# Kernel optimization log

Hardware: AMD Instinct MI355X
Metric: run time of the kernel (lower is better)

Reference implementation:

```python
import jax, jax.numpy as jnp
import numpy as np

E, H, M, IN, T = 4, 64, 64, 32, 32      # e_size, hidden_state, message, in_size, target
HL = (128, 256, 128)                     # NNet hidden layers (priba's NNet default)
N_LAYERS = 3


def setup_inputs() -> dict:
    key = jax.random.key(0)
    ks = iter(jax.random.split(key, 64))
    B, N = 16, 128

    def w(shape, scale=0.1):
        return jax.random.normal(next(ks), shape, dtype=jnp.float32) * scale

    inp = {
        "h_in": jax.random.normal(next(ks), (B, N, IN), dtype=jnp.float32),
        "am": jax.random.normal(next(ks), (B, N, N, E), dtype=jnp.float32),
        "g_size": jax.random.randint(next(ks), (B,), 0, N),
    }
    # EdgeNetwork NNet: E -> 128 -> 256 -> 128 -> M*H
    dims_e = (E,) + HL + (M * H,)
    for i in range(4):
        inp[f"We{i}"] = w((dims_e[i], dims_e[i + 1]))
        inp[f"be{i}"] = w((dims_e[i + 1],))
    # GRU (torch nn.GRU, one layer, one step): input M, hidden H
    inp["Wih"] = w((3 * H, M)); inp["Whh"] = w((3 * H, H))
    inp["bih"] = w((3 * H,)); inp["bhh"] = w((3 * H,))
    # Readout NNets: i on [h_T, h_0] (H+IN -> T), j on h_T (H -> T)
    dims_i = (H + IN,) + HL + (T,)
    dims_j = (H,) + HL + (T,)
    for i in range(4):
        inp[f"Wi{i}"] = w((dims_i[i], dims_i[i + 1])); inp[f"bi{i}"] = w((dims_i[i + 1],))
        inp[f"Wj{i}"] = w((dims_j[i], dims_j[i + 1])); inp[f"bj{i}"] = w((dims_j[i + 1],))
    return inp


def _mlp(x, Ws, bs):
    for Wk, bk in zip(Ws[:-1], bs[:-1]):
        x = jax.nn.relu(x @ Wk + bk)
    return x @ Ws[-1] + bs[-1]


def reference(h_in, am, g_size,
              We0, be0, We1, be1, We2, be2, We3, be3,
              Wih, Whh, bih, bhh,
              Wi0, bi0, Wi1, bi1, Wi2, bi2, Wi3, bi3,
              Wj0, bj0, Wj1, bj1, Wj2, bj2, Wj3, bj3):
    B, N, _ = h_in.shape
    h = jnp.pad(h_in, ((0, 0), (0, 0), (0, H - IN)))            # pad to hidden size
    mask = (jnp.arange(N)[None, :] < g_size[:, None]).astype(h.dtype)[:, :, None]  # [B,N,1]

    # Edge-network hidden features; final linear layer is fused into the
    # message contraction to avoid materializing per-edge [M,H] matrices.
    f = am                                                       # [B,N,N,E]
    for Wk, bk in ((We0, be0), (We1, be1), (We2, be2)):
        f = jax.nn.relu(f @ Wk + bk)                             # [B,N,N,128]
    W3 = We3.reshape(HL[-1], M, H)                               # [128,M,H]
    b3 = be3.reshape(M, H)

    for _ in range(N_LAYERS):                                    # weight-tied GGNN steps
        # m[b,v,o] = sum_w (A(e_bvw) @ h_bw)[o], A = reshape(f @ We3 + be3)
        t = jnp.einsum('bvwk,bwi->bvki', f, h)                   # [B,N,128,H]
        msg = jnp.einsum('bvki,koi->bvo', t, W3)
        msg = msg + jnp.einsum('oi,bi->bo', b3, h.sum(1))[:, None, :]
        # single-step torch GRU update
        gi = msg @ Wih.T + bih
        gh = h @ Whh.T + bhh
        r = jax.nn.sigmoid(gi[..., :H] + gh[..., :H])
        z = jax.nn.sigmoid(gi[..., H:2 * H] + gh[..., H:2 * H])
        n = jnp.tanh(gi[..., 2 * H:] + r * gh[..., 2 * H:])
        h = (1.0 - z) * n + z * h
        h = h * mask

    # GGNN readout: sum_v mask * sigmoid(i([h_T, h_0])) * j(h_T), then log_softmax
    gate = jax.nn.sigmoid(_mlp(jnp.concatenate([h, h_in], -1),
                               (Wi0, Wi1, Wi2, Wi3), (bi0, bi1, bi2, bi3)))
    val = _mlp(h, (Wj0, Wj1, Wj2, Wj3), (bj0, bj1, bj2, bj3))
    res = (mask * gate * val).sum(1)                             # [B,T]
    return jax.nn.log_softmax(res, axis=1)
```

## Files before the change

### kernel.cpp

```cpp
#include <hip/hip_runtime.h>
#include <math.h>

#define B   16
#define N   128
#define E   4
#define H   64
#define M   64
#define IN_ 32
#define T   32
#define K1  128
#define K2  256
#define K3  128

typedef _Float16 f16;
typedef f16  f16x8 __attribute__((ext_vector_type(8)));
typedef float f32x4 __attribute__((ext_vector_type(4)));

#define MFMA16(a, b, c) __builtin_amdgcn_mfma_f32_16x16x32_f16(a, b, c, 0, 0, 0)

#define OFF_W1T   0
#define OFF_W2T   32768
#define OFF_WE3H  65536
#define OFF_RI0   589824
#define OFF_RI1   602112
#define OFF_RI2   634880
#define OFF_RI3   667648
#define OFF_RJ0   671744
#define OFF_RJ1   679936
#define OFF_RJ2   712704
#define OFF_RJ3   745472
#define WPACK_SZ  749568

__global__ __launch_bounds__(256) void pad_h_kernel(const float* __restrict__ h_in,
                                                    float* __restrict__ h,
                                                    f16* __restrict__ h16,
                                                    f16* __restrict__ hin16) {
    int idx = blockIdx.x * 256 + threadIdx.x;
    if (idx >= B * N * H) return;
    int i  = idx & (H - 1);
    int bn = idx >> 6;
    float v = (i < IN_) ? h_in[bn * IN_ + i] : 0.f;
    h[idx] = v;
    h16[idx] = (f16)v;
    if (i < IN_) hin16[bn * IN_ + i] = (f16)v;
}

__global__ __launch_bounds__(256) void prep_weights(
    const float* __restrict__ We1, const float* __restrict__ We2,
    const float* __restrict__ We3,
    const float* __restrict__ Wi0, const float* __restrict__ Wi1,
    const float* __restrict__ Wi2, const float* __restrict__ Wi3,
    const float* __restrict__ Wj0, const float* __restrict__ Wj1,
    const float* __restrict__ Wj2, const float* __restrict__ Wj3,
    f16* __restrict__ wp) {
    int idx = blockIdx.x * 256 + threadIdx.x;
    if (idx < OFF_W2T) {
        int t = idx;
        int j = t >> 7, k = t & 127;
        wp[idx] = (f16)We1[k * 256 + j];
    } else if (idx < OFF_WE3H) {
        int t = idx - OFF_W2T;
        int j = t >> 8, k = t & 255;
        wp[idx] = (f16)We2[k * 128 + j];
    } else if (idx < OFF_RI0) {
        int t = idx - OFF_WE3H;
        wp[idx] = (f16)We3[t];
    } else if (idx < OFF_RI1) {
        int t = idx - OFF_RI0;
        int n = t / 96, c = t % 96;
        wp[idx] = (f16)Wi0[c * 128 + n];
    } else if (idx < OFF_RI2) {
        int t = idx - OFF_RI1;
        int n = t >> 7, k = t & 127;
        wp[idx] = (f16)Wi1[k * 256 + n];
    } else if (idx < OFF_RI3) {
        int t = idx - OFF_RI2;
        int n = t >> 8, k = t & 255;
        wp[idx] = (f16)Wi2[k * 128 + n];
    } else if (idx < OFF_RJ0) {
        int t = idx - OFF_RI3;
        int n = t >> 7, k = t & 127;
        wp[idx] = (f16)Wi3[k * 32 + n];
    } else if (idx < OFF_RJ1) {
        int t = idx - OFF_RJ0;
        int n = t >> 6, c = t & 63;
        wp[idx] = (f16)Wj0[c * 128 + n];
    } else if (idx < OFF_RJ2) {
        int t = idx - OFF_RJ1;
        int n = t >> 7, k = t & 127;
        wp[idx] = (f16)Wj1[k * 256 + n];
    } else if (idx < OFF_RJ3) {
        int t = idx - OFF_RJ2;
        int n = t >> 8, k = t & 255;
        wp[idx] = (f16)Wj2[k * 128 + n];
    } else if (idx < WPACK_SZ) {
        int t = idx - OFF_RJ3;
        int n = t >> 7, k = t & 127;
        wp[idx] = (f16)Wj3[k * 32 + n];
    }
}

__global__ __launch_bounds__(256, 2) void edge_mlp_mfma(
    const float* __restrict__ am,
    const float* __restrict__ We0, const float* __restrict__ be0,
    const f16* __restrict__ W1t, const float* __restrict__ be1,
    const f16* __restrict__ W2t, const float* __restrict__ be2,
    f16* __restrict__ f) {
    __shared__ float xl[64][4];
    __shared__ f16 y1[64][136];
    __shared__ f16 y2[64][264];
    int tid = threadIdx.x;
    int lane = tid & 63, wv = tid >> 6;
    long long g0 = (long long)blockIdx.x * 64;

    ((float*)xl)[tid] = am[g0 * 4 + tid];
    __syncthreads();

    {
        int j = tid & 127, e0 = (tid >> 7) * 32;
        float w0 = We0[j], w1 = We0[128 + j], w2 = We0[256 + j], w3 = We0[384 + j];
        float bb = be0[j];
        #pragma unroll 8
        for (int e = e0; e < e0 + 32; ++e) {
            float v = bb + xl[e][0] * w0 + xl[e][1] * w1
                         + xl[e][2] * w2 + xl[e][3] * w3;
            y1[e][j] = (f16)fmaxf(v, 0.f);
        }
    }
    __syncthreads();

    int m = lane & 15, q = lane >> 4;

    {
        f32x4 acc[4][4];
        #pragma unroll
        for (int ct = 0; ct < 4; ++ct)
            #pragma unroll
            for (int rt = 0; rt < 4; ++rt) acc[ct][rt] = (f32x4){0.f, 0.f, 0.f, 0.f};
        #pragma unroll
        for (int s = 0; s < 4; ++s) {
            int k0 = s * 32 + q * 8;
            f16x8 afr[4], bfr[4];
            #pragma unroll
            for (int rt = 0; rt < 4; ++rt)
                afr[rt] = *(const f16x8*)&y1[rt * 16 + m][k0];
            #pragma unroll
            for (int ct = 0; ct < 4; ++ct) {
                int n = (wv * 4 + ct) * 16 + m;
                bfr[ct] = *(const f16x8*)(W1t + n * 128 + k0);
            }
            #pragma unroll
            for (int ct = 0; ct < 4; ++ct)
                #pragma unroll
                for (int rt = 0; rt < 4; ++rt)
                    acc[ct][rt] = MFMA16(afr[rt], bfr[ct], acc[ct][rt]);
        }
        #pragma unroll
        for (int ct = 0; ct < 4; ++ct) {
            int n = (wv * 4 + ct) * 16 + m;
            float bb = be1[n];
            #pragma unroll
            for (int rt = 0; rt < 4; ++rt)
                #pragma unroll
                for (int r = 0; r < 4; ++r) {
                    int row = rt * 16 + q * 4 + r;
                    y2[row][n] = (f16)fmaxf(acc[ct][rt][r] + bb, 0.f);
                }
        }
    }
    __syncthreads();

    {
        f32x4 acc[2][4];
        #pragma unroll
        for (int ct = 0; ct < 2; ++ct)
            #pragma unroll
            for (int rt = 0; rt < 4; ++rt) acc[ct][rt] = (f32x4){0.f, 0.f, 0.f, 0.f};
        #pragma unroll
        for (int s = 0; s < 8; ++s) {
            int k0 = s * 32 + q * 8;
            f16x8 afr[4], bfr[2];
            #pragma unroll
            for (int rt = 0; rt < 4; ++rt)
                afr[rt] = *(const f16x8*)&y2[rt * 16 + m][k0];
            #pragma unroll
            for (int ct = 0; ct < 2; ++ct) {
                int n = (wv * 2 + ct) * 16 + m;
                bfr[ct] = *(const f16x8*)(W2t + n * 256 + k0);
            }
            #pragma unroll
            for (int ct = 0; ct < 2; ++ct)
                #pragma unroll
                for (int rt = 0; rt < 4; ++rt)
                    acc[ct][rt] = MFMA16(afr[rt], bfr[ct], acc[ct][rt]);
        }
        #pragma unroll
        for (int ct = 0; ct < 2; ++ct) {
            int n = (wv * 2 + ct) * 16 + m;
            float bb = be2[n];
            #pragma unroll
            for (int rt = 0; rt < 4; ++rt)
                #pragma unroll
                for (int r = 0; r < 4; ++r) {
                    int row = rt * 16 + q * 4 + r;
                    y1[row][n] = (f16)fmaxf(acc[ct][rt][r] + bb, 0.f);
                }
        }
    }
    __syncthreads();

    #pragma unroll
    for (int j = 0; j < 4; ++j) {
        int c = tid + j * 256;
        int e = c >> 4, p = c & 15;
        *(uint4*)(f + (g0 + e) * 128 + p * 8) = *(const uint4*)&y1[e][p * 8];
    }
}

__global__ __launch_bounds__(256) void msg_init_kernel(
    const float* __restrict__ h, const float* __restrict__ be3,
    float* __restrict__ msgb) {
    __shared__ float part[4][64];
    __shared__ float hsum[64];
    __shared__ float bias[64];
    int tid = threadIdx.x;
    int b = blockIdx.x;
    int i = tid & 63, wq = tid >> 6;
    float s = 0.f;
    for (int w = wq; w < N; w += 4) s += h[((size_t)(b * N + w)) * H + i];
    part[wq][i] = s;
    __syncthreads();
    if (tid < 64) hsum[tid] = part[0][tid] + part[1][tid] + part[2][tid] + part[3][tid];
    __syncthreads();
    if (tid < 64) {
        float sb = 0.f;
        #pragma unroll 4
        for (int ii = 0; ii < H; ++ii) sb += be3[tid * H + ii] * hsum[ii];
        bias[tid] = sb;
    }
    __syncthreads();
    for (int idx = tid; idx < N * M; idx += 256)
        msgb[(size_t)b * N * M + idx] = bias[idx & 63];
}

__global__ __launch_bounds__(256, 2) void p_gemm(
    const f16* __restrict__ h16, const f16* __restrict__ We3h,
    f16* __restrict__ P2) {
    __shared__ f16 Al[128][72];
    __shared__ f16 Bl[128][72];
    __shared__ f16 Ol[128][136];
    int tid = threadIdx.x, lane = tid & 63, wv = tid >> 6;
    int ob = blockIdx.x;
    int nt = blockIdx.y;

    #pragma unroll
    for (int j = 0; j < 4; ++j) {
        int c = tid + j * 256;
        int row = c >> 3, p = c & 7;
        *(uint4*)&Al[row][p * 8] =
            *(const uint4*)(h16 + (size_t)(nt * 128 + row) * 64 + p * 8);
    }
    #pragma unroll
    for (int j = 0; j < 4; ++j) {
        int c = tid + j * 256;
        int k = c >> 3, p = c & 7;
        *(uint4*)&Bl[k][p * 8] =
            *(const uint4*)(We3h + ((size_t)(k * 64 + ob)) * 64 + p * 8);
    }
    __syncthreads();

    int m = lane & 15, q = lane >> 4;
    f32x4 acc[2][8];
    #pragma unroll
    for (int ct = 0; ct < 2; ++ct)
        #pragma unroll
        for (int rt = 0; rt < 8; ++rt) acc[ct][rt] = (f32x4){0.f, 0.f, 0.f, 0.f};
    #pragma unroll
    for (int s = 0; s < 2; ++s) {
        int k0 = s * 32 + q * 8;
        f16x8 afr[8], bfr[2];
        #pragma unroll
        for (int rt = 0; rt < 8; ++rt)
            afr[rt] = *(const f16x8*)&Al[rt * 16 + m][k0];
        #pragma unroll
        for (int ct = 0; ct < 2; ++ct)
            bfr[ct] = *(const f16x8*)&Bl[(wv * 2 + ct) * 16 + m][k0];
        #pragma unroll
        for (int ct = 0; ct < 2; ++ct)
            #pragma unroll
            for (int rt = 0; rt < 8; ++rt)
                acc[ct][rt] = MFMA16(afr[rt], bfr[ct], acc[ct][rt]);
    }
    #pragma unroll
    for (int ct = 0; ct < 2; ++ct) {
        int col = (wv * 2 + ct) * 16 + m;
        #pragma unroll
        for (int rt = 0; rt < 8; ++rt)
            #pragma unroll
            for (int r = 0; r < 4; ++r)
                Ol[rt * 16 + q * 4 + r][col] = (f16)acc[ct][rt][r];
    }
    __syncthreads();
    #pragma unroll
    for (int j = 0; j < 8; ++j) {
        int c = tid + j * 256;
        int row = c >> 4, p = c & 15;
        *(uint4*)(P2 + ((size_t)(nt * 128 + row) * 64 + ob) * 128 + p * 8) =
            *(const uint4*)&Ol[row][p * 8];
    }
}

__global__ __launch_bounds__(256, 2) void msg_mfma(
    const f16* __restrict__ f, const f16* __restrict__ P2,
    float* __restrict__ part) {
    __shared__ f16 Al[128][136];
    __shared__ f16 Bl[64][136];
    int tid = threadIdx.x, lane = tid & 63, wv = tid >> 6;
    int ws = blockIdx.x;
    int b  = blockIdx.y;
    int m = lane & 15, q = lane >> 4;

    f32x4 acc[2][4];
    #pragma unroll
    for (int rt = 0; rt < 2; ++rt)
        #pragma unroll
        for (int ct = 0; ct < 4; ++ct) acc[rt][ct] = (f32x4){0.f, 0.f, 0.f, 0.f};

    for (int wi = 0; wi < 4; ++wi) {
        int w = ws * 4 + wi;
        #pragma unroll
        for (int j = 0; j < 8; ++j) {
            int c = tid + j * 256;
            int v = c >> 4, p = c & 15;
            *(uint4*)&Al[v][p * 8] =
                *(const uint4*)(f + (((size_t)(b * 128 + v) * 128 + w) * 128) + p * 8);
        }
        #pragma unroll
        for (int j = 0; j < 4; ++j) {
            int c = tid + j * 256;
            int o = c >> 4, p = c & 15;
            *(uint4*)&Bl[o][p * 8] =
                *(const uint4*)(P2 + (((size_t)(b * 128 + w) * 64 + o) * 128) + p * 8);
        }
        __syncthreads();
        #pragma unroll
        for (int s = 0; s < 4; ++s) {
            int k0 = s * 32 + q * 8;
            f16x8 afr[2], bfr[4];
            #pragma unroll
            for (int rt = 0; rt < 2; ++rt)
                afr[rt] = *(const f16x8*)&Al[(wv * 2 + rt) * 16 + m][k0];
            #pragma unroll
            for (int ct = 0; ct < 4; ++ct)
                bfr[ct] = *(const f16x8*)&Bl[ct * 16 + m][k0];
            #pragma unroll
            for (int rt = 0; rt < 2; ++rt)
                #pragma unroll
                for (int ct = 0; ct < 4; ++ct)
                    acc[rt][ct] = MFMA16(afr[rt], bfr[ct], acc[rt][ct]);
        }
        __syncthreads();
    }
    float* pp = part + (size_t)ws * (2048 * 64);
    #pragma unroll
    for (int rt = 0; rt < 2; ++rt)
        #pragma unroll
        for (int ct = 0; ct < 4; ++ct) {
            int o = ct * 16 + m;
            #pragma unroll
            for (int r = 0; r < 4; ++r) {
                int v = (wv * 2 + rt) * 16 + q * 4 + r;
                pp[(size_t)(b * 128 + v) * 64 + o] = acc[rt][ct][r];
            }
        }
}

__global__ __launch_bounds__(192) void gru_kernel(
    const float* __restrict__ msgb, const float* __restrict__ part,
    float* __restrict__ h, f16* __restrict__ h16,
    const float* __restrict__ Wih, const float* __restrict__ Whh,
    const float* __restrict__ bih, const float* __restrict__ bhh,
    const int* __restrict__ g_size) {
    __shared__ float m_lds[M];
    __shared__ float h_lds[H];
    __shared__ float gi[3 * H], gh[3 * H];
    int tid = threadIdx.x;
    int bv  = blockIdx.x;
    int b = bv >> 7, v = bv & 127;

    if (tid < M) {
        float s = msgb[bv * M + tid];
        #pragma unroll 8
        for (int sp = 0; sp < 32; ++sp)
            s += part[(size_t)sp * (2048 * 64) + bv * 64 + tid];
        m_lds[tid] = s;
    } else if (tid < M + H) {
        h_lds[tid - M] = h[bv * H + (tid - M)];
    }
    __syncthreads();

    {
        float si = bih[tid], sh = bhh[tid];
        const float* wi = Wih + tid * M;
        const float* wh = Whh + tid * H;
        #pragma unroll 4
        for (int k = 0; k < M; ++k) si += wi[k] * m_lds[k];
        #pragma unroll 4
        for (int k = 0; k < H; ++k) sh += wh[k] * h_lds[k];
        gi[tid] = si;
        gh[tid] = sh;
    }
    __syncthreads();
    if (tid < H) {
        float r = 1.f / (1.f + expf(-(gi[tid] + gh[tid])));
        float z = 1.f / (1.f + expf(-(gi[H + tid] + gh[H + tid])));
        float n = tanhf(gi[2 * H + tid] + r * gh[2 * H + tid]);
        float hv = (1.f - z) * n + z * h_lds[tid];
        float maskf = (v < g_size[b]) ? 1.f : 0.f;
        hv *= maskf;
        h[bv * H + tid] = hv;
        h16[bv * H + tid] = (f16)hv;
    }
}

__global__ __launch_bounds__(256, 4) void readout_mfma(
    const f16* __restrict__ h16, const f16* __restrict__ hin16,
    const int* __restrict__ g_size,
    const f16* __restrict__ Ri0, const float* __restrict__ bi0,
    const f16* __restrict__ Ri1, const float* __restrict__ bi1,
    const f16* __restrict__ Ri2, const float* __restrict__ bi2,
    const f16* __restrict__ Ri3, const float* __restrict__ bi3,
    const f16* __restrict__ Rj0, const float* __restrict__ bj0,
    const f16* __restrict__ Rj1, const float* __restrict__ bj1,
    const f16* __restrict__ Rj2, const float* __restrict__ bj2,
    const f16* __restrict__ Rj3, const float* __restrict__ bj3,
    float* __restrict__ contrib) {
    __shared__ f16 Xl[32][104];
    __shared__ f16 A1[32][136];
    __shared__ f16 A2[32][264];
    __shared__ float Gl[32][36];
    int tid = threadIdx.x, lane = tid & 63, wv = tid >> 6;
    int m = lane & 15, q = lane >> 4;
    int r0 = blockIdx.x * 32;

    {
        int row = tid >> 3, p = tid & 7;
        *(uint4*)&Xl[row][p * 8] = *(const uint4*)(h16 + (size_t)(r0 + row) * 64 + p * 8);
        if (tid < 128) {
            int row2 = tid >> 2, p2 = tid & 3;
            *(uint4*)&Xl[row2][64 + p2 * 8] =
                *(const uint4*)(hin16 + (size_t)(r0 + row2) * 32 + p2 * 8);
        }
    }
    __syncthreads();

    {
        f32x4 acc[2][2];
        #pragma unroll
        for (int ct = 0; ct < 2; ++ct)
            #pragma unroll
            for (int rt = 0; rt < 2; ++rt) acc[ct][rt] = (f32x4){0.f, 0.f, 0.f, 0.f};
        #pragma unroll
        for (int s = 0; s < 3; ++s) {
            int k0 = s * 32 + q * 8;
            f16x8 afr[2], bfr[2];
            #pragma unroll
            for (int rt = 0; rt < 2; ++rt) afr[rt] = *(const f16x8*)&Xl[rt * 16 + m][k0];
            #pragma unroll
            for (int ct = 0; ct < 2; ++ct)
                bfr[ct] = *(const f16x8*)(Ri0 + ((wv * 2 + ct) * 16 + m) * 96 + k0);
            #pragma unroll
            for (int ct = 0; ct < 2; ++ct)
                #pragma unroll
                for (int rt = 0; rt < 2; ++rt)
                    acc[ct][rt] = MFMA16(afr[rt], bfr[ct], acc[ct][rt]);
        }
        #pragma unroll
        for (int ct = 0; ct < 2; ++ct) {
            int n = (wv * 2 + ct) * 16 + m;
            float bb = bi0[n];
            #pragma unroll
            for (int rt = 0; rt < 2; ++rt)
                #pragma unroll
                for (int r = 0; r < 4; ++r)
                    A1[rt * 16 + q * 4 + r][n] = (f16)fmaxf(acc[ct][rt][r] + bb, 0.f);
        }
    }
    __syncthreads();

    {
        f32x4 acc[4][2];
        #pragma unroll
        for (int ct = 0; ct < 4; ++ct)
            #pragma unroll
            for (int rt = 0; rt < 2; ++rt) acc[ct][rt] = (f32x4){0.f, 0.f, 0.f, 0.f};
        #pragma unroll
        for (int s = 0; s < 4; ++s) {
            int k0 = s * 32 + q * 8;
            f16x8 afr[2], bfr[4];
            #pragma unroll
            for (int rt = 0; rt < 2; ++rt) afr[rt] = *(const f16x8*)&A1[rt * 16 + m][k0];
            #pragma unroll
            for (int ct = 0; ct < 4; ++ct)
                bfr[ct] = *(const f16x8*)(Ri1 + ((wv * 4 + ct) * 16 + m) * 128 + k0);
            #pragma unroll
            for (int ct = 0; ct < 4; ++ct)
                #pragma unroll
                for (int rt = 0; rt < 2; ++rt)
                    acc[ct][rt] = MFMA16(afr[rt], bfr[ct], acc[ct][rt]);
        }
        #pragma unroll
        for (int ct = 0; ct < 4; ++ct) {
            int n = (wv * 4 + ct) * 16 + m;
            float bb = bi1[n];
            #pragma unroll
            for (int rt = 0; rt < 2; ++rt)
                #pragma unroll
                for (int r = 0; r < 4; ++r)
                    A2[rt * 16 + q * 4 + r][n] = (f16)fmaxf(acc[ct][rt][r] + bb, 0.f);
        }
    }
    __syncthreads();

    {
        f32x4 acc[2][2];
        #pragma unroll
        for (int ct = 0; ct < 2; ++ct)
            #pragma unroll
            for (int rt = 0; rt < 2; ++rt) acc[ct][rt] = (f32x4){0.f, 0.f, 0.f, 0.f};
        #pragma unroll
        for (int s = 0; s < 8; ++s) {
            int k0 = s * 32 + q * 8;
            f16x8 afr[2], bfr[2];
            #pragma unroll
            for (int rt = 0; rt < 2; ++rt) afr[rt] = *(const f16x8*)&A2[rt * 16 + m][k0];
            #pragma unroll
            for (int ct = 0; ct < 2; ++ct)
                bfr[ct] = *(const f16x8*)(Ri2 + ((wv * 2 + ct) * 16 + m) * 256 + k0);
            #pragma unroll
            for (int ct = 0; ct < 2; ++ct)
                #pragma unroll
                for (int rt = 0; rt < 2; ++rt)
                    acc[ct][rt] = MFMA16(afr[rt], bfr[ct], acc[ct][rt]);
        }
        __syncthreads();
        #pragma unroll
        for (int ct = 0; ct < 2; ++ct) {
            int n = (wv * 2 + ct) * 16 + m;
            float bb = bi2[n];
            #pragma unroll
            for (int rt = 0; rt < 2; ++rt)
                #pragma unroll
                for (int r = 0; r < 4; ++r)
                    A1[rt * 16 + q * 4 + r][n] = (f16)fmaxf(acc[ct][rt][r] + bb, 0.f);
        }
    }
    __syncthreads();

    if (wv < 2) {
        f32x4 acc[2];
        acc[0] = (f32x4){0.f, 0.f, 0.f, 0.f};
        acc[1] = (f32x4){0.f, 0.f, 0.f, 0.f};
        int n = wv * 16 + m;
        #pragma unroll
        for (int s = 0; s < 4; ++s) {
            int k0 = s * 32 + q * 8;
            f16x8 bfr = *(const f16x8*)(Ri3 + n * 128 + k0);
            #pragma unroll
            for (int rt = 0; rt < 2; ++rt) {
                f16x8 afr = *(const f16x8*)&A1[rt * 16 + m][k0];
                acc[rt] = MFMA16(afr, bfr, acc[rt]);
            }
        }
        float bb = bi3[n];
        #pragma unroll
        for (int rt = 0; rt < 2; ++rt)
            #pragma unroll
            for (int r = 0; r < 4; ++r)
                Gl[rt * 16 + q * 4 + r][n] = 1.f / (1.f + expf(-(acc[rt][r] + bb)));
    }
    __syncthreads();

    {
        f32x4 acc[2][2];
        #pragma unroll
        for (int ct = 0; ct < 2; ++ct)
            #pragma unroll
            for (int rt = 0; rt < 2; ++rt) acc[ct][rt] = (f32x4){0.f, 0.f, 0.f, 0.f};
        #pragma unroll
        for (int s = 0; s < 2; ++s) {
            int k0 = s * 32 + q * 8;
            f16x8 afr[2], bfr[2];
            #pragma unroll
            for (int rt = 0; rt < 2; ++rt) afr[rt] = *(const f16x8*)&Xl[rt * 16 + m][k0];
            #pragma unroll
            for (int ct = 0; ct < 2; ++ct)
                bfr[ct] = *(const f16x8*)(Rj0 + ((wv * 2 + ct) * 16 + m) * 64 + k0);
            #pragma unroll
            for (int ct = 0; ct < 2; ++ct)
                #pragma unroll
                for (int rt = 0; rt < 2; ++rt)
                    acc[ct][rt] = MFMA16(afr[rt], bfr[ct], acc[ct][rt]);
        }
        __syncthreads();
        #pragma unroll
        for (int ct = 0; ct < 2; ++ct) {
            int n = (wv * 2 + ct) * 16 + m;
            float bb = bj0[n];
            #pragma unroll
            for (int rt = 0; rt < 2; ++rt)
                #pragma unroll
                for (int r = 0; r < 4; ++r)
                    A1[rt * 16 + q * 4 + r][n] = (f16)fmaxf(acc[ct][rt][r] + bb, 0.f);
        }
    }
    __syncthreads();

    {
        f32x4 acc[4][2];
        #pragma unroll
        for (int ct = 0; ct < 4; ++ct)
            #pragma unroll
            for (int rt = 0; rt < 2; ++rt) acc[ct][rt] = (f32x4){0.f, 0.f, 0.f, 0.f};
        #pragma unroll
        for (int s = 0; s < 4; ++s) {
            int k0 = s * 32 + q * 8;
            f16x8 afr[2], bfr[4];
            #pragma unroll
            for (int rt = 0; rt < 2; ++rt) afr[rt] = *(const f16x8*)&A1[rt * 16 + m][k0];
            #pragma unroll
            for (int ct = 0; ct < 4; ++ct)
                bfr[ct] = *(const f16x8*)(Rj1 + ((wv * 4 + ct) * 16 + m) * 128 + k0);
            #pragma unroll
            for (int ct = 0; ct < 4; ++ct)
                #pragma unroll
                for (int rt = 0; rt < 2; ++rt)
                    acc[ct][rt] = MFMA16(afr[rt], bfr[ct], acc[ct][rt]);
        }
        #pragma unroll
        for (int ct = 0; ct < 4; ++ct) {
            int n = (wv * 4 + ct) * 16 + m;
            float bb = bj1[n];
            #pragma unroll
            for (int rt = 0; rt < 2; ++rt)
                #pragma unroll
                for (int r = 0; r < 4; ++r)
                    A2[rt * 16 + q * 4 + r][n] = (f16)fmaxf(acc[ct][rt][r] + bb, 0.f);
        }
    }
    __syncthreads();

    {
        f32x4 acc[2][2];
        #pragma unroll
        for (int ct = 0; ct < 2; ++ct)
            #pragma unroll
            for (int rt = 0; rt < 2; ++rt) acc[ct][rt] = (f32x4){0.f, 0.f, 0.f, 0.f};
        #pragma unroll
        for (int s = 0; s < 8; ++s) {
            int k0 = s * 32 + q * 8;
            f16x8 afr[2], bfr[2];
            #pragma unroll
            for (int rt = 0; rt < 2; ++rt) afr[rt] = *(const f16x8*)&A2[rt * 16 + m][k0];
            #pragma unroll
            for (int ct = 0; ct < 2; ++ct)
                bfr[ct] = *(const f16x8*)(Rj2 + ((wv * 2 + ct) * 16 + m) * 256 + k0);
            #pragma unroll
            for (int ct = 0; ct < 2; ++ct)
                #pragma unroll
                for (int rt = 0; rt < 2; ++rt)
                    acc[ct][rt] = MFMA16(afr[rt], bfr[ct], acc[ct][rt]);
        }
        __syncthreads();
        #pragma unroll
        for (int ct = 0; ct < 2; ++ct) {
            int n = (wv * 2 + ct) * 16 + m;
            float bb = bj2[n];
            #pragma unroll
            for (int rt = 0; rt < 2; ++rt)
                #pragma unroll
                for (int r = 0; r < 4; ++r)
                    A1[rt * 16 + q * 4 + r][n] = (f16)fmaxf(acc[ct][rt][r] + bb, 0.f);
        }
    }
    __syncthreads();

    if (wv < 2) {
        f32x4 acc[2];
        acc[0] = (f32x4){0.f, 0.f, 0.f, 0.f};
        acc[1] = (f32x4){0.f, 0.f, 0.f, 0.f};
        int n = wv * 16 + m;
        #pragma unroll
        for (int s = 0; s < 4; ++s) {
            int k0 = s * 32 + q * 8;
            f16x8 bfr = *(const f16x8*)(Rj3 + n * 128 + k0);
            #pragma unroll
            for (int rt = 0; rt < 2; ++rt) {
                f16x8 afr = *(const f16x8*)&A1[rt * 16 + m][k0];
                acc[rt] = MFMA16(afr, bfr, acc[rt]);
            }
        }
        float bb = bj3[n];
        #pragma unroll
        for (int rt = 0; rt < 2; ++rt)
            #pragma unroll
            for (int r = 0; r < 4; ++r) {
                int row = rt * 16 + q * 4 + r;
                int rg = r0 + row;
                int b = rg >> 7, v = rg & 127;
                float maskf = (v < g_size[b]) ? 1.f : 0.f;
                contrib[(size_t)rg * T + n] = maskf * Gl[row][n] * (acc[rt][r] + bb);
            }
    }
}

__global__ __launch_bounds__(64) void finalize_kernel(const float* __restrict__ contrib,
                                                      float* __restrict__ out) {
    __shared__ float res[T];
    int b = blockIdx.x;
    int o = threadIdx.x;
    if (o < T) {
        float s = 0.f;
        for (int v = 0; v < N; ++v) s += contrib[(b * N + v) * T + o];
        res[o] = s;
    }
    __syncthreads();
    if (o < T) {
        float mx = res[0];
        for (int i = 1; i < T; ++i) mx = fmaxf(mx, res[i]);
        float se = 0.f;
        for (int i = 0; i < T; ++i) se += expf(res[i] - mx);
        out[b * T + o] = res[o] - mx - logf(se);
    }
}

extern "C" void kernel_launch(void* const* d_in, const int* in_sizes, int n_in,
                              void* d_out, int out_size, void* d_ws, size_t ws_size,
                              hipStream_t stream) {
    (void)in_sizes; (void)n_in; (void)out_size; (void)ws_size;
    const float* h_in = (const float*)d_in[0];
    const float* am   = (const float*)d_in[1];
    const int*   g_sz = (const int*)d_in[2];
    const float* We0 = (const float*)d_in[3],  *be0 = (const float*)d_in[4];
    const float* We1 = (const float*)d_in[5],  *be1 = (const float*)d_in[6];
    const float* We2 = (const float*)d_in[7],  *be2 = (const float*)d_in[8];
    const float* We3 = (const float*)d_in[9],  *be3 = (const float*)d_in[10];
    const float* Wih = (const float*)d_in[11], *Whh = (const float*)d_in[12];
    const float* bih = (const float*)d_in[13], *bhh = (const float*)d_in[14];
    const float* Wi0 = (const float*)d_in[15], *bi0 = (const float*)d_in[16];
    const float* Wj0 = (const float*)d_in[17], *bj0 = (const float*)d_in[18];
    const float* Wi1 = (const float*)d_in[19], *bi1 = (const float*)d_in[20];
    const float* Wj1 = (const float*)d_in[21], *bj1 = (const float*)d_in[22];
    const float* Wi2 = (const float*)d_in[23], *bi2 = (const float*)d_in[24];
    const float* Wj2 = (const float*)d_in[25], *bj2 = (const float*)d_in[26];
    const float* Wi3 = (const float*)d_in[27], *bi3 = (const float*)d_in[28];
    const float* Wj3 = (const float*)d_in[29], *bj3 = (const float*)d_in[30];

    float* out = (float*)d_out;

    f16*   f    = (f16*)d_ws;
    f16*   P2   = f + (size_t)33554432;
    float* part = (float*)(P2 + (size_t)16777216);
    float* h    = part + (size_t)4194304;
    float* msgb = h + 131072;
    float* contrib = msgb + 131072;
    f16*   h16  = (f16*)(contrib + 65536);
    f16*   hin16 = h16 + 131072;
    f16*   wp   = hin16 + 65536;

    f16* W1t  = wp + OFF_W1T;
    f16* W2t  = wp + OFF_W2T;
    f16* We3h = wp + OFF_WE3H;
    f16* Ri0  = wp + OFF_RI0;
    f16* Ri1  = wp + OFF_RI1;
    f16* Ri2  = wp + OFF_RI2;
    f16* Ri3  = wp + OFF_RI3;
    f16* Rj0  = wp + OFF_RJ0;
    f16* Rj1  = wp + OFF_RJ1;
    f16* Rj2  = wp + OFF_RJ2;
    f16* Rj3  = wp + OFF_RJ3;

    pad_h_kernel<<<(B * N * H) / 256, 256, 0, stream>>>(h_in, h, h16, hin16);
    prep_weights<<<WPACK_SZ / 256, 256, 0, stream>>>(We1, We2, We3,
                                                     Wi0, Wi1, Wi2, Wi3,
                                                     Wj0, Wj1, Wj2, Wj3, wp);
    edge_mlp_mfma<<<(B * N * N) / 64, 256, 0, stream>>>(am, We0, be0, W1t, be1,
                                                        W2t, be2, f);
    for (int l = 0; l < 3; ++l) {
        msg_init_kernel<<<B, 256, 0, stream>>>(h, be3, msgb);
        p_gemm<<<dim3(64, 16), 256, 0, stream>>>(h16, We3h, P2);
        msg_mfma<<<dim3(32, 16), 256, 0, stream>>>(f, P2, part);
        gru_kernel<<<B * N, 192, 0, stream>>>(msgb, part, h, h16,
                                              Wih, Whh, bih, bhh, g_sz);
    }
    readout_mfma<<<64, 256, 0, stream>>>(h16, hin16, g_sz,
                                         Ri0, bi0, Ri1, bi1, Ri2, bi2, Ri3, bi3,
                                         Rj0, bj0, Rj1, bj1, Rj2, bj2, Rj3, bj3,
                                         contrib);
    finalize_kernel<<<B, 64, 0, stream>>>(contrib, out);
}
```

Measured before the change: 414.7 us.

## Merge prep kernels and co-schedule edge MLP, P-GEMM and bias blocks

Merges the h padding and weight packing into one prep kernel. Runs the edge MLP, the first layer's P-GEMM and the message bias reduction as disjoint block ranges of a single mega kernel that shares a union of shared-memory layouts. Replaces the per-node broadcast bias buffer with a per-graph [B,64] bias read directly by the GRU. The aim is fewer launches, filling the tail of the edge MLP with independent work, and dropping the msgb broadcast writes. The shared-memory union takes the size of the largest member, which may limit occupancy for the smaller roles.

```diff
diff --git a/kernel.cpp b/kernel.cpp
--- a/kernel.cpp
+++ b/kernel.cpp
@@ -31,40 +31,41 @@
 #define OFF_RJ3   745472
 #define WPACK_SZ  749568
 
-__global__ __launch_bounds__(256) void pad_h_kernel(const float* __restrict__ h_in,
-                                                    float* __restrict__ h,
-                                                    f16* __restrict__ h16,
-                                                    f16* __restrict__ hin16) {
-    int idx = blockIdx.x * 256 + threadIdx.x;
-    if (idx >= B * N * H) return;
-    int i  = idx & (H - 1);
-    int bn = idx >> 6;
-    float v = (i < IN_) ? h_in[bn * IN_ + i] : 0.f;
-    h[idx] = v;
-    h16[idx] = (f16)v;
-    if (i < IN_) hin16[bn * IN_ + i] = (f16)v;
-}
-
-__global__ __launch_bounds__(256) void prep_weights(
+union SmemU {
+    struct { float xl[64][4]; f16 y1[64][136]; f16 y2[64][264]; } e;
+    struct { f16 Al[128][72]; f16 Bl[128][72]; f16 Ol[128][136]; } pg;
+    struct { float prt[4][64]; float hsum[64]; float bias[64]; } bi;
+};
+
+__global__ __launch_bounds__(256) void prep_kernel(
+    const float* __restrict__ h_in,
     const float* __restrict__ We1, const float* __restrict__ We2,
     const float* __restrict__ We3,
     const float* __restrict__ Wi0, const float* __restrict__ Wi1,
     const float* __restrict__ Wi2, const float* __restrict__ Wi3,
     const float* __restrict__ Wj0, const float* __restrict__ Wj1,
     const float* __restrict__ Wj2, const float* __restrict__ Wj3,
+    float* __restrict__ h, f16* __restrict__ h16, f16* __restrict__ hin16,
     f16* __restrict__ wp) {
     int idx = blockIdx.x * 256 + threadIdx.x;
+    if (idx < B * N * H) {
+        int i  = idx & (H - 1);
+        int bn = idx >> 6;
+        float v = (i < IN_) ? h_in[bn * IN_ + i] : 0.f;
+        h[idx] = v;
+        h16[idx] = (f16)v;
+        if (i < IN_) hin16[bn * IN_ + i] = (f16)v;
+    }
+    if (idx >= WPACK_SZ) return;
     if (idx < OFF_W2T) {
-        int t = idx;
-        int j = t >> 7, k = t & 127;
+        int j = idx >> 7, k = idx & 127;
         wp[idx] = (f16)We1[k * 256 + j];
     } else if (idx < OFF_WE3H) {
         int t = idx - OFF_W2T;
         int j = t >> 8, k = t & 255;
         wp[idx] = (f16)We2[k * 128 + j];
     } else if (idx < OFF_RI0) {
-        int t = idx - OFF_WE3H;
-        wp[idx] = (f16)We3[t];
+        wp[idx] = (f16)We3[idx - OFF_WE3H];
     } else if (idx < OFF_RI1) {
         int t = idx - OFF_RI0;
         int n = t / 96, c = t % 96;
@@ -93,27 +94,27 @@
         int t = idx - OFF_RJ2;
         int n = t >> 8, k = t & 255;
         wp[idx] = (f16)Wj2[k * 128 + n];
-    } else if (idx < WPACK_SZ) {
+    } else {
         int t = idx - OFF_RJ3;
         int n = t >> 7, k = t & 127;
         wp[idx] = (f16)Wj3[k * 32 + n];
     }
 }
 
-__global__ __launch_bounds__(256, 2) void edge_mlp_mfma(
-    const float* __restrict__ am,
-    const float* __restrict__ We0, const float* __restrict__ be0,
-    const f16* __restrict__ W1t, const float* __restrict__ be1,
-    const f16* __restrict__ W2t, const float* __restrict__ be2,
-    f16* __restrict__ f) {
-    __shared__ float xl[64][4];
-    __shared__ f16 y1[64][136];
-    __shared__ f16 y2[64][264];
-    int tid = threadIdx.x;
+
+__device__ void edge_body(SmemU& su, int tid, int tile,
+                          const float* __restrict__ am,
+                          const float* __restrict__ We0,
+                          const float* __restrict__ be0,
+                          const f16* __restrict__ W1t,
+                          const float* __restrict__ be1,
+                          const f16* __restrict__ W2t,
+                          const float* __restrict__ be2,
+                          f16* __restrict__ f) {
     int lane = tid & 63, wv = tid >> 6;
-    long long g0 = (long long)blockIdx.x * 64;
-
-    ((float*)xl)[tid] = am[g0 * 4 + tid];
+    long long g0 = (long long)tile * 64;
+
+    ((float*)su.e.xl)[tid] = am[g0 * 4 + tid];
     __syncthreads();
 
     {
@@ -122,9 +123,9 @@
         float bb = be0[j];
         #pragma unroll 8
         for (int e = e0; e < e0 + 32; ++e) {
-            float v = bb + xl[e][0] * w0 + xl[e][1] * w1
-                         + xl[e][2] * w2 + xl[e][3] * w3;
-            y1[e][j] = (f16)fmaxf(v, 0.f);
+            float v = bb + su.e.xl[e][0] * w0 + su.e.xl[e][1] * w1
+                         + su.e.xl[e][2] * w2 + su.e.xl[e][3] * w3;
+            su.e.y1[e][j] = (f16)fmaxf(v, 0.f);
         }
     }
     __syncthreads();
@@ -143,7 +144,7 @@
             f16x8 afr[4], bfr[4];
             #pragma unroll
             for (int rt = 0; rt < 4; ++rt)
-                afr[rt] = *(const f16x8*)&y1[rt * 16 + m][k0];
+                afr[rt] = *(const f16x8*)&su.e.y1[rt * 16 + m][k0];
             #pragma unroll
             for (int ct = 0; ct < 4; ++ct) {
                 int n = (wv * 4 + ct) * 16 + m;
@@ -164,7 +165,7 @@
                 #pragma unroll
                 for (int r = 0; r < 4; ++r) {
                     int row = rt * 16 + q * 4 + r;
-                    y2[row][n] = (f16)fmaxf(acc[ct][rt][r] + bb, 0.f);
+                    su.e.y2[row][n] = (f16)fmaxf(acc[ct][rt][r] + bb, 0.f);
                 }
         }
     }
@@ -182,7 +183,7 @@
             f16x8 afr[4], bfr[2];
             #pragma unroll
             for (int rt = 0; rt < 4; ++rt)
-                afr[rt] = *(const f16x8*)&y2[rt * 16 + m][k0];
+                afr[rt] = *(const f16x8*)&su.e.y2[rt * 16 + m][k0];
             #pragma unroll
             for (int ct = 0; ct < 2; ++ct) {
                 int n = (wv * 2 + ct) * 16 + m;
@@ -203,7 +204,7 @@
                 #pragma unroll
                 for (int r = 0; r < 4; ++r) {
                     int row = rt * 16 + q * 4 + r;
-                    y1[row][n] = (f16)fmaxf(acc[ct][rt][r] + bb, 0.f);
+                    su.e.y1[row][n] = (f16)fmaxf(acc[ct][rt][r] + bb, 0.f);
                 }
         }
     }
@@ -212,60 +213,30 @@
     #pragma unroll
     for (int j = 0; j < 4; ++j) {
         int c = tid + j * 256;
-        int e = c >> 4, p = c & 15;
-        *(uint4*)(f + (g0 + e) * 128 + p * 8) = *(const uint4*)&y1[e][p * 8];
-    }
-}
-
-__global__ __launch_bounds__(256) void msg_init_kernel(
-    const float* __restrict__ h, const float* __restrict__ be3,
-    float* __restrict__ msgb) {
-    __shared__ float part[4][64];
-    __shared__ float hsum[64];
-    __shared__ float bias[64];
-    int tid = threadIdx.x;
-    int b = blockIdx.x;
-    int i = tid & 63, wq = tid >> 6;
-    float s = 0.f;
-    for (int w = wq; w < N; w += 4) s += h[((size_t)(b * N + w)) * H + i];
-    part[wq][i] = s;
-    __syncthreads();
-    if (tid < 64) hsum[tid] = part[0][tid] + part[1][tid] + part[2][tid] + part[3][tid];
-    __syncthreads();
-    if (tid < 64) {
-        float sb = 0.f;
-        #pragma unroll 4
-        for (int ii = 0; ii < H; ++ii) sb += be3[tid * H + ii] * hsum[ii];
-        bias[tid] = sb;
-    }
-    __syncthreads();
-    for (int idx = tid; idx < N * M; idx += 256)
-        msgb[(size_t)b * N * M + idx] = bias[idx & 63];
-}
-
-__global__ __launch_bounds__(256, 2) void p_gemm(
-    const f16* __restrict__ h16, const f16* __restrict__ We3h,
-    f16* __restrict__ P2) {
-    __shared__ f16 Al[128][72];
-    __shared__ f16 Bl[128][72];
-    __shared__ f16 Ol[128][136];
-    int tid = threadIdx.x, lane = tid & 63, wv = tid >> 6;
-    int ob = blockIdx.x;
-    int nt = blockIdx.y;
+        int e = c >> 4, pp = c & 15;
+        *(uint4*)(f + (g0 + e) * 128 + pp * 8) = *(const uint4*)&su.e.y1[e][pp * 8];
+    }
+}
+
+__device__ void pgemm_body(SmemU& su, int tid, int ob, int nt,
+                           const f16* __restrict__ h16,
+                           const f16* __restrict__ We3h,
+                           f16* __restrict__ P2) {
+    int lane = tid & 63, wv = tid >> 6;
 
     #pragma unroll
     for (int j = 0; j < 4; ++j) {
         int c = tid + j * 256;
-        int row = c >> 3, p = c & 7;
-        *(uint4*)&Al[row][p * 8] =
-            *(const uint4*)(h16 + (size_t)(nt * 128 + row) * 64 + p * 8);
+        int row = c >> 3, pp = c & 7;
+        *(uint4*)&su.pg.Al[row][pp * 8] =
+            *(const uint4*)(h16 + (size_t)(nt * 128 + row) * 64 + pp * 8);
     }
     #pragma unroll
     for (int j = 0; j < 4; ++j) {
         int c = tid + j * 256;
-        int k = c >> 3, p = c & 7;
-        *(uint4*)&Bl[k][p * 8] =
-            *(const uint4*)(We3h + ((size_t)(k * 64 + ob)) * 64 + p * 8);
+        int k = c >> 3, pp = c & 7;
+        *(uint4*)&su.pg.Bl[k][pp * 8] =
+            *(const uint4*)(We3h + ((size_t)(k * 64 + ob)) * 64 + pp * 8);
     }
     __syncthreads();
 
@@ -281,10 +252,10 @@
         f16x8 afr[8], bfr[2];
         #pragma unroll
         for (int rt = 0; rt < 8; ++rt)
-            afr[rt] = *(const f16x8*)&Al[rt * 16 + m][k0];
+            afr[rt] = *(const f16x8*)&su.pg.Al[rt * 16 + m][k0];
         #pragma unroll
         for (int ct = 0; ct < 2; ++ct)
-            bfr[ct] = *(const f16x8*)&Bl[(wv * 2 + ct) * 16 + m][k0];
+            bfr[ct] = *(const f16x8*)&su.pg.Bl[(wv * 2 + ct) * 16 + m][k0];
         #pragma unroll
         for (int ct = 0; ct < 2; ++ct)
             #pragma unroll
@@ -298,15 +269,72 @@
         for (int rt = 0; rt < 8; ++rt)
             #pragma unroll
             for (int r = 0; r < 4; ++r)
-                Ol[rt * 16 + q * 4 + r][col] = (f16)acc[ct][rt][r];
+                su.pg.Ol[rt * 16 + q * 4 + r][col] = (f16)acc[ct][rt][r];
     }
     __syncthreads();
     #pragma unroll
     for (int j = 0; j < 8; ++j) {
         int c = tid + j * 256;
-        int row = c >> 4, p = c & 15;
-        *(uint4*)(P2 + ((size_t)(nt * 128 + row) * 64 + ob) * 128 + p * 8) =
-            *(const uint4*)&Ol[row][p * 8];
+        int row = c >> 4, pp = c & 15;
+        *(uint4*)(P2 + ((size_t)(nt * 128 + row) * 64 + ob) * 128 + pp * 8) =
+            *(const uint4*)&su.pg.Ol[row][pp * 8];
+    }
+}
+
+__device__ void bias_body(SmemU& su, int tid, int b,
+                          const float* __restrict__ h,
+                          const float* __restrict__ be3,
+                          float* __restrict__ biasb) {
+    int i = tid & 63, wq = tid >> 6;
+    float s = 0.f;
+    for (int w = wq; w < N; w += 4) s += h[((size_t)(b * N + w)) * H + i];
+    su.bi.prt[wq][i] = s;
+    __syncthreads();
+    if (tid < 64)
+        su.bi.hsum[tid] = su.bi.prt[0][tid] + su.bi.prt[1][tid]
+                        + su.bi.prt[2][tid] + su.bi.prt[3][tid];
+    __syncthreads();
+    if (tid < 64) {
+        float sb = 0.f;
+        #pragma unroll 4
+        for (int ii = 0; ii < H; ++ii) sb += be3[tid * H + ii] * su.bi.hsum[ii];
+        biasb[b * 64 + tid] = sb;
+    }
+}
+
+__global__ __launch_bounds__(256, 2) void mega0_kernel(
+    const float* __restrict__ am,
+    const float* __restrict__ We0, const float* __restrict__ be0,
+    const float* __restrict__ be1, const float* __restrict__ be2,
+    const float* __restrict__ be3,
+    const f16* __restrict__ wp,
+    const float* __restrict__ h, const f16* __restrict__ h16,
+    f16* __restrict__ f, f16* __restrict__ P2, float* __restrict__ biasb) {
+    __shared__ SmemU su;
+    int tid = threadIdx.x;
+    int bid = blockIdx.x;
+    if (bid < 4096) {
+        edge_body(su, tid, bid, am, We0, be0, wp + OFF_W1T, be1, wp + OFF_W2T,
+                  be2, f);
+    } else if (bid < 5120) {
+        int t = bid - 4096;
+        pgemm_body(su, tid, t & 63, t >> 6, h16, wp + OFF_WE3H, P2);
+    } else {
+        bias_body(su, tid, bid - 5120, h, be3, biasb);
+    }
+}
+
+__global__ __launch_bounds__(256, 2) void pg_bias_kernel(
+    const float* __restrict__ be3, const f16* __restrict__ wp,
+    const float* __restrict__ h, const f16* __restrict__ h16,
+    f16* __restrict__ P2, float* __restrict__ biasb) {
+    __shared__ SmemU su;
+    int tid = threadIdx.x;
+    int bid = blockIdx.x;
+    if (bid < 1024) {
+        pgemm_body(su, tid, bid & 63, bid >> 6, h16, wp + OFF_WE3H, P2);
+    } else {
+        bias_body(su, tid, bid - 1024, h, be3, biasb);
     }
 }
 
@@ -331,16 +359,16 @@
         #pragma unroll
         for (int j = 0; j < 8; ++j) {
             int c = tid + j * 256;
-            int v = c >> 4, p = c & 15;
-            *(uint4*)&Al[v][p * 8] =
-                *(const uint4*)(f + (((size_t)(b * 128 + v) * 128 + w) * 128) + p * 8);
+            int v = c >> 4, pp = c & 15;
+            *(uint4*)&Al[v][pp * 8] =
+                *(const uint4*)(f + (((size_t)(b * 128 + v) * 128 + w) * 128) + pp * 8);
         }
         #pragma unroll
         for (int j = 0; j < 4; ++j) {
             int c = tid + j * 256;
-            int o = c >> 4, p = c & 15;
-            *(uint4*)&Bl[o][p * 8] =
-                *(const uint4*)(P2 + (((size_t)(b * 128 + w) * 64 + o) * 128) + p * 8);
+            int o = c >> 4, pp = c & 15;
+            *(uint4*)&Bl[o][pp * 8] =
+                *(const uint4*)(P2 + (((size_t)(b * 128 + w) * 64 + o) * 128) + pp * 8);
         }
         __syncthreads();
         #pragma unroll
@@ -376,7 +404,7 @@
 }
 
 __global__ __launch_bounds__(192) void gru_kernel(
-    const float* __restrict__ msgb, const float* __restrict__ part,
+    const float* __restrict__ biasb, const float* __restrict__ part,
     float* __restrict__ h, f16* __restrict__ h16,
     const float* __restrict__ Wih, const float* __restrict__ Whh,
     const float* __restrict__ bih, const float* __restrict__ bhh,
@@ -389,7 +417,7 @@
     int b = bv >> 7, v = bv & 127;
 
     if (tid < M) {
-        float s = msgb[bv * M + tid];
+        float s = biasb[b * 64 + tid];
         #pragma unroll 8
         for (int sp = 0; sp < 32; ++sp)
             s += part[(size_t)sp * (2048 * 64) + bv * 64 + tid];
@@ -425,27 +453,27 @@
 
 __global__ __launch_bounds__(256, 4) void readout_mfma(
     const f16* __restrict__ h16, const f16* __restrict__ hin16,
-    const int* __restrict__ g_size,
-    const f16* __restrict__ Ri0, const float* __restrict__ bi0,
-    const f16* __restrict__ Ri1, const float* __restrict__ bi1,
-    const f16* __restrict__ Ri2, const float* __restrict__ bi2,
-    const f16* __restrict__ Ri3, const float* __restrict__ bi3,
-    const f16* __restrict__ Rj0, const float* __restrict__ bj0,
-    const f16* __restrict__ Rj1, const float* __restrict__ bj1,
-    const f16* __restrict__ Rj2, const float* __restrict__ bj2,
-    const f16* __restrict__ Rj3, const float* __restrict__ bj3,
+    const int* __restrict__ g_size, const f16* __restrict__ wp,
+    const float* __restrict__ bi0, const float* __restrict__ bi1,
+    const float* __restrict__ bi2, const float* __restrict__ bi3,
+    const float* __restrict__ bj0, const float* __restrict__ bj1,
+    const float* __restrict__ bj2, const float* __restrict__ bj3,
     float* __restrict__ contrib) {
     __shared__ f16 Xl[32][104];
     __shared__ f16 A1[32][136];
     __shared__ f16 A2[32][264];
     __shared__ float Gl[32][36];
+    const f16* Ri0 = wp + OFF_RI0; const f16* Ri1 = wp + OFF_RI1;
+    const f16* Ri2 = wp + OFF_RI2; const f16* Ri3 = wp + OFF_RI3;
+    const f16* Rj0 = wp + OFF_RJ0; const f16* Rj1 = wp + OFF_RJ1;
+    const f16* Rj2 = wp + OFF_RJ2; const f16* Rj3 = wp + OFF_RJ3;
     int tid = threadIdx.x, lane = tid & 63, wv = tid >> 6;
     int m = lane & 15, q = lane >> 4;
     int r0 = blockIdx.x * 32;
 
     {
-        int row = tid >> 3, p = tid & 7;
-        *(uint4*)&Xl[row][p * 8] = *(const uint4*)(h16 + (size_t)(r0 + row) * 64 + p * 8);
+        int row = tid >> 3, pp = tid & 7;
+        *(uint4*)&Xl[row][pp * 8] = *(const uint4*)(h16 + (size_t)(r0 + row) * 64 + pp * 8);
         if (tid < 128) {
             int row2 = tid >> 2, p2 = tid & 3;
             *(uint4*)&Xl[row2][64 + p2 * 8] =
@@ -762,40 +790,31 @@
     f16*   P2   = f + (size_t)33554432;
     float* part = (float*)(P2 + (size_t)16777216);
     float* h    = part + (size_t)4194304;
-    float* msgb = h + 131072;
-    float* contrib = msgb + 131072;
+    float* biasb = h + 131072;
+    float* contrib = biasb + 1024;
     f16*   h16  = (f16*)(contrib + 65536);
     f16*   hin16 = h16 + 131072;
     f16*   wp   = hin16 + 65536;
 
-    f16* W1t  = wp + OFF_W1T;
-    f16* W2t  = wp + OFF_W2T;
-    f16* We3h = wp + OFF_WE3H;
-    f16* Ri0  = wp + OFF_RI0;
-    f16* Ri1  = wp + OFF_RI1;
-    f16* Ri2  = wp + OFF_RI2;
-    f16* Ri3  = wp + OFF_RI3;
-    f16* Rj0  = wp + OFF_RJ0;
-    f16* Rj1  = wp + OFF_RJ1;
-    f16* Rj2  = wp + OFF_RJ2;
-    f16* Rj3  = wp + OFF_RJ3;
-
-    pad_h_kernel<<<(B * N * H) / 256, 256, 0, stream>>>(h_in, h, h16, hin16);
-    prep_weights<<<WPACK_SZ / 256, 256, 0, stream>>>(We1, We2, We3,
-                                                     Wi0, Wi1, Wi2, Wi3,
-                                                     Wj0, Wj1, Wj2, Wj3, wp);
-    edge_mlp_mfma<<<(B * N * N) / 64, 256, 0, stream>>>(am, We0, be0, W1t, be1,
-                                                        W2t, be2, f);
-    for (int l = 0; l < 3; ++l) {
-        msg_init_kernel<<<B, 256, 0, stream>>>(h, be3, msgb);
-        p_gemm<<<dim3(64, 16), 256, 0, stream>>>(h16, We3h, P2);
+    prep_kernel<<<(WPACK_SZ + 255) / 256, 256, 0, stream>>>(
+        h_in, We1, We2, We3, Wi0, Wi1, Wi2, Wi3, Wj0, Wj1, Wj2, Wj3,
+        h, h16, hin16, wp);
+
+    mega0_kernel<<<4096 + 1024 + 16, 256, 0, stream>>>(
+        am, We0, be0, be1, be2, be3, wp, h, h16, f, P2, biasb);
+    msg_mfma<<<dim3(32, 16), 256, 0, stream>>>(f, P2, part);
+    gru_kernel<<<B * N, 192, 0, stream>>>(biasb, part, h, h16,
+                                          Wih, Whh, bih, bhh, g_sz);
+
+    for (int l = 1; l < 3; ++l) {
+        pg_bias_kernel<<<1024 + 16, 256, 0, stream>>>(be3, wp, h, h16, P2, biasb);
         msg_mfma<<<dim3(32, 16), 256, 0, stream>>>(f, P2, part);
-        gru_kernel<<<B * N, 192, 0, stream>>>(msgb, part, h, h16,
+        gru_kernel<<<B * N, 192, 0, stream>>>(biasb, part, h, h16,
                                               Wih, Whh, bih, bhh, g_sz);
     }
-    readout_mfma<<<64, 256, 0, stream>>>(h16, hin16, g_sz,
-                                         Ri0, bi0, Ri1, bi1, Ri2, bi2, Ri3, bi3,
-                                         Rj0, bj0, Rj1, bj1, Rj2, bj2, Rj3, bj3,
-                                         contrib);
+
+    readout_mfma<<<64, 256, 0, stream>>>(h16, hin16, g_sz, wp,
+                                         bi0, bi1, bi2, bi3,
+                                         bj0, bj1, bj2, bj3, contrib);
     finalize_kernel<<<B, 64, 0, stream>>>(contrib, out);
 }
```

Measured after the change: 412.1 us. About the same (-0.6%).
